# Kernel tuning notes

Hardware: AMD Instinct MI355X
Metric: run time of the kernel (lower is better)

## Reference

```python
import jax, jax.numpy as jnp
import numpy as np

# Connected-components labeling via iterative 4-neighbor min-label propagation.
# Label VALUES differ from tfa.image.connected_components' sequential numbering,
# but component memberships (and hence unique_with_counts -> max count) are identical.

def _mode_count(fg):
    # fg: [H, W] bool, True = foreground. Returns int32 = max count among unique
    # labels of the flattened label image (background label 0 included, as in the
    # original unique_with_counts over the full flattened labeling).
    H, W = fg.shape
    n = H * W
    big = jnp.int32(n + 1)  # sentinel larger than any real label
    init = jnp.where(fg, jnp.arange(1, n + 1, dtype=jnp.int32).reshape(H, W), 0)

    def prop(lbl):
        l = jnp.where(fg, lbl, big)
        up = jnp.concatenate([jnp.full((1, W), big, jnp.int32), l[:-1]], axis=0)
        down = jnp.concatenate([l[1:], jnp.full((1, W), big, jnp.int32)], axis=0)
        left = jnp.concatenate([jnp.full((H, 1), big, jnp.int32), l[:, :-1]], axis=1)
        right = jnp.concatenate([l[:, 1:], jnp.full((H, 1), big, jnp.int32)], axis=1)
        m = jnp.minimum(l, jnp.minimum(jnp.minimum(up, down), jnp.minimum(left, right)))
        return jnp.where(fg, m, 0).astype(jnp.int32)

    def cond(st):
        prev, cur = st
        return jnp.any(prev != cur)

    def body(st):
        _, cur = st
        return (cur, prop(cur))

    _, labels = jax.lax.while_loop(cond, body, (init, prop(init)))
    counts = jnp.zeros(n + 1, jnp.int32).at[labels.reshape(-1)].add(1)
    return jnp.max(counts)


def setup_inputs() -> dict:
    key = jax.random.key(0)
    # [n_color_distances, n_boxes, batch, n_patches, H, W], binary 0/1
    x = jax.random.randint(key, (3, 5, 32, 64, 32, 32), 0, 2).astype(jnp.float32)
    return {"x": x}


def reference(x) -> jnp.ndarray:
    C, B, Bt, P, H, W = x.shape
    fg = (x != 0).reshape(-1, H, W)                      # [C*B*Bt*P, H, W]
    counts = jax.vmap(_mode_count)(fg).reshape(C, B, Bt, P)
    # tf.reduce_mean on an integer tensor truncates (integer division)
    perc = (jnp.sum(counts, axis=-1) // P).astype(jnp.float32)  # [C, B, Bt]
    return perc
```

## Files before the change

### kernel.cpp

```cpp
#include <hip/hip_runtime.h>
#include <stdint.h>


#define N_IMGS 30720
#define N_OUT  480
#define WAVES_PER_BLOCK 4
#define IMGS_PER_BLOCK (WAVES_PER_BLOCK * 2)

__device__ __forceinline__ int findH(int* L, int i) {
    for (;;) {
        int p = L[i] & 511;
        if (p == i) return i;
        int g = L[p] & 511;
        if (g == p) return p;
        L[i] = g;
        i = g;
    }
}

__global__ __launch_bounds__(256, 8)
void ccl_wave2_kernel(const uint32_t* __restrict__ x, int* __restrict__ maxc) {
    __shared__ int Lbuf[IMGS_PER_BLOCK * 512];

    const int lane = threadIdx.x & 63;
    const int wv   = threadIdx.x >> 6;
    const int half = lane >> 5;
    const int row  = lane & 31;
    const size_t img = (size_t)blockIdx.x * IMGS_PER_BLOCK + wv * 2 + half;
    int* L = Lbuf + (wv * 2 + half) * 512;

    const size_t pairBase = ((size_t)blockIdx.x * IMGS_PER_BLOCK + wv * 2) * 1024;
    const uint4* wp = (const uint4*)(x + pairBase) + lane;
    uint32_t W = 0;
    #pragma unroll
    for (int j = 0; j < 8; ++j) {
        uint4 q = wp[j * 64];
        uint32_t n = (q.x >> 29) | ((q.y >> 29) << 1)
                   | ((q.z >> 29) << 2) | ((q.w >> 29) << 3);
        W |= n << (4 * j);
    }

    const int slBase = (lane & 7) * 8;
    const int jsh    = (lane >> 3) * 4;
    uint32_t m = 0;
    #pragma unroll
    for (int t = 0; t < 8; ++t) {
        uint32_t sv = (uint32_t)__shfl((int)W, slBase + t);
        m |= ((sv >> jsh) & 0xFu) << (4 * t);
    }

    uint32_t runStarts = m & ~(m << 1);
    int nruns = __popc(runStarts);
    int packed = nruns | (__popc(m) << 16);
    int scan = packed;
    #pragma unroll
    for (int off = 1; off < 64; off <<= 1) {
        int u = __shfl_up(scan, off);
        if (lane >= off) scan += u;
    }
    const int totalA   = __shfl(scan, 31);
    const int totalAll = __shfl(scan, 63);
    const int myTotal  = half ? (totalAll - totalA) : totalA;
    const int base = (scan - packed - (half ? totalA : 0)) & 0xFFFF;
    const int R    = myTotal & 0xFFFF;
    const int fg   = myTotal >> 16;

    for (int i = row; i < R; i += 32) L[i] = i;

    uint32_t mprev  = __shfl_up(m, 1);
    uint32_t rsPrev = __shfl_up(runStarts, 1);
    int      bPrev  = __shfl_up(base, 1);
    if (row == 0) mprev = 0;
    uint32_t ov  = m & mprev;
    uint32_t ovs = ov & ~(ov << 1);

    int lastA = -1, rootA = -1;
    int lastB = -1, rootB = -1;
    while (ovs) {
        int c = __ffs(ovs) - 1; ovs &= ovs - 1;
        uint32_t mc = (2u << c) - 1;
        int a = base  + __popc(runStarts & mc) - 1;
        int b = bPrev + __popc(rsPrev    & mc) - 1;

        int ra = (a == lastA) ? rootA : a;
        int rb = (b == lastB) ? rootB : b;
        for (;;) {
            int pa = L[ra] & 511;
            int pb = L[rb] & 511;
            if (pa == ra && pb == rb) break;
            int ga = L[pa] & 511;
            int gb = L[pb] & 511;
            if (pa != ra) { L[ra] = ga; ra = ga; }
            if (pb != rb) { L[rb] = gb; rb = gb; }
        }
        while (ra != rb) {
            int hi = ra > rb ? ra : rb;
            int lo = ra ^ rb ^ hi;
            int old = atomicCAS(&L[hi], hi, lo);
            if (old == hi) { ra = lo; break; }
            ra = findH(L, old & 511);
            rb = lo;
        }
        lastA = a; rootA = ra; lastB = b; rootB = ra;
    }

    uint32_t mm = m;
    int idx = base;
    while (mm) {
        int s = __ffs(mm) - 1;
        uint32_t t  = mm + (1u << s);
        uint32_t rm = (t ^ mm) & mm;
        mm &= ~rm;
        int r0 = L[idx] & 511;
        int r1 = L[r0] & 511;
        if (r1 != r0) r1 = findH(L, r1);
        atomicAdd(&L[r1], __popc(rm) << 9);
        ++idx;
    }

    int mx = 0;
    for (int i = row; i < R; i += 32) {
        int v = L[i];
        if ((v & 511) == i) mx = max(mx, v >> 9);
    }
    #pragma unroll
    for (int off = 1; off < 32; off <<= 1) mx = max(mx, __shfl_xor(mx, off));

    if (row == 0) maxc[img] = max(mx, 1024 - fg);
}

__global__ __launch_bounds__(64)
void patch_reduce_kernel(const int* __restrict__ maxc, float* __restrict__ out) {
    const int o = blockIdx.x;
    int v = maxc[(size_t)o * 64 + threadIdx.x];
    #pragma unroll
    for (int off = 32; off > 0; off >>= 1)
        v += __shfl_down(v, off);
    if (threadIdx.x == 0) out[o] = (float)(v >> 6);
}

extern "C" void kernel_launch(void* const* d_in, const int* in_sizes, int n_in,
                              void* d_out, int out_size, void* d_ws, size_t ws_size,
                              hipStream_t stream) {
    const uint32_t* x = (const uint32_t*)d_in[0];
    float* out = (float*)d_out;
    int* maxc = (int*)d_ws;

    ccl_wave2_kernel<<<N_IMGS / IMGS_PER_BLOCK, 256, 0, stream>>>(x, maxc);
    patch_reduce_kernel<<<N_OUT, 64, 0, stream>>>(maxc, out);
}
```

Baseline: 189.6 us.

## Store run sizes with labels at init and accumulate counts per label entry

Each union-find entry is now set up with its own run length packed into the upper bits. Path compression and the union CAS keep those count bits intact. After merging, two rounds of pointer jumping flatten the forest, then each non-root entry adds its count into its root, replacing the per-run walk that added counts with atomics. Blocks shrink from 4 waves to 2 and the occupancy hint is dropped. This changes atomic traffic and how parallel the final pass is, but adds extra compression passes and a read before each CAS.

Result: no change. 191.1 us (+0.8%).

```diff
diff --git a/kernel.cpp b/kernel.cpp
--- a/kernel.cpp
+++ b/kernel.cpp
@@ -4,21 +4,22 @@
 
 #define N_IMGS 30720
 #define N_OUT  480
-#define WAVES_PER_BLOCK 4
+#define WAVES_PER_BLOCK 2
 #define IMGS_PER_BLOCK (WAVES_PER_BLOCK * 2)
 
 __device__ __forceinline__ int findH(int* L, int i) {
     for (;;) {
-        int p = L[i] & 511;
+        int v = L[i];
+        int p = v & 511;
         if (p == i) return i;
         int g = L[p] & 511;
         if (g == p) return p;
-        L[i] = g;
+        L[i] = g | (v & ~511);
         i = g;
     }
 }
 
-__global__ __launch_bounds__(256, 8)
+__global__ __launch_bounds__(128)
 void ccl_wave2_kernel(const uint32_t* __restrict__ x, int* __restrict__ maxc) {
     __shared__ int Lbuf[IMGS_PER_BLOCK * 512];
 
@@ -65,7 +66,18 @@
     const int R    = myTotal & 0xFFFF;
     const int fg   = myTotal >> 16;
 
-    for (int i = row; i < R; i += 32) L[i] = i;
+    {
+        uint32_t mm = m;
+        int idx = base;
+        while (mm) {
+            int s = __ffs(mm) - 1;
+            uint32_t t  = mm + (1u << s);
+            uint32_t rm = (t ^ mm) & mm;
+            mm &= ~rm;
+            L[idx] = idx | (__popc(rm) << 9);
+            ++idx;
+        }
+    }
 
     uint32_t mprev  = __shfl_up(m, 1);
     uint32_t rsPrev = __shfl_up(runStarts, 1);
@@ -85,37 +97,46 @@
         int ra = (a == lastA) ? rootA : a;
         int rb = (b == lastB) ? rootB : b;
         for (;;) {
-            int pa = L[ra] & 511;
-            int pb = L[rb] & 511;
+            int va = L[ra], vb = L[rb];
+            int pa = va & 511, pb = vb & 511;
             if (pa == ra && pb == rb) break;
             int ga = L[pa] & 511;
             int gb = L[pb] & 511;
-            if (pa != ra) { L[ra] = ga; ra = ga; }
-            if (pb != rb) { L[rb] = gb; rb = gb; }
+            if (pa != ra) { L[ra] = ga | (va & ~511); ra = ga; }
+            if (pb != rb) { L[rb] = gb | (vb & ~511); rb = gb; }
         }
         while (ra != rb) {
             int hi = ra > rb ? ra : rb;
             int lo = ra ^ rb ^ hi;
-            int old = atomicCAS(&L[hi], hi, lo);
-            if (old == hi) { ra = lo; break; }
-            ra = findH(L, old & 511);
+            int cur = L[hi];
+            if ((cur & 511) == hi) {
+                int old = atomicCAS(&L[hi], cur, lo | (cur & ~511));
+                if (old == cur) { ra = lo; break; }
+                cur = old;
+            }
+            ra = findH(L, cur & 511);
             rb = lo;
         }
         lastA = a; rootA = ra; lastB = b; rootB = ra;
     }
 
-    uint32_t mm = m;
-    int idx = base;
-    while (mm) {
-        int s = __ffs(mm) - 1;
-        uint32_t t  = mm + (1u << s);
-        uint32_t rm = (t ^ mm) & mm;
-        mm &= ~rm;
-        int r0 = L[idx] & 511;
-        int r1 = L[r0] & 511;
-        if (r1 != r0) r1 = findH(L, r1);
-        atomicAdd(&L[r1], __popc(rm) << 9);
-        ++idx;
+    #pragma unroll
+    for (int rnd = 0; rnd < 2; ++rnd) {
+        for (int i = row; i < R; i += 32) {
+            int v = L[i];
+            int p = v & 511;
+            int g = L[p] & 511;
+            if (g != p) L[i] = g | (v & ~511);
+        }
+    }
+
+    for (int i = row; i < R; i += 32) {
+        int v = L[i];
+        int r = v & 511;
+        if (r == i) continue;
+        int p = L[r] & 511;
+        if (p != r) r = findH(L, p);
+        atomicAdd(&L[r], v & ~511);
     }
 
     int mx = 0;
@@ -146,6 +167,6 @@
     float* out = (float*)d_out;
     int* maxc = (int*)d_ws;
 
-    ccl_wave2_kernel<<<N_IMGS / IMGS_PER_BLOCK, 256, 0, stream>>>(x, maxc);
+    ccl_wave2_kernel<<<N_IMGS / IMGS_PER_BLOCK, 128, 0, stream>>>(x, maxc);
     patch_reduce_kernel<<<N_OUT, 64, 0, stream>>>(maxc, out);
 }
```
